# Kernel tuning notes

Hardware: AMD Instinct MI355X
Metric: run time of the kernel (lower is better)

Reference implementation:

```python
import jax, jax.numpy as jnp
from jax import lax
import numpy as np


def setup_inputs() -> dict:
    key = jax.random.key(0)
    k1, k2 = jax.random.split(key)
    sat_features = jax.random.normal(k1, (128, 4, 64, 16), dtype=jnp.float32)  # [B_s, h, w, c]
    grd_features = jax.random.normal(k2, (128, 4, 64, 16), dtype=jnp.float32)  # [B_g, h, gw, c]
    return {"sat_features": sat_features, "grd_features": grd_features}


def reference(sat_features, grd_features):
    B_s, h, w, c = sat_features.shape
    B_g, gh, gw, gc = grd_features.shape
    assert h == gh and c == gc

    # --- corr: circular cross-correlation over width via conv2d ---
    n = gw - 1
    sat_pad = jnp.concatenate([sat_features, sat_features[:, :, :n, :]], axis=2)  # [B_s,h,w+n,c]
    rhs = jnp.transpose(grd_features, (1, 2, 3, 0))  # HWIO: [h,gw,c,B_g]
    out = lax.conv_general_dilated(
        sat_pad, rhs, window_strides=(1, 1), padding='VALID',
        dimension_numbers=('NHWC', 'HWIO', 'NHWC'))  # [B_s,1,w,B_g]
    corr = out[:, 0, :, :]                  # [B_s, w, B_g]
    orien = jnp.argmax(corr, axis=1)        # [B_s, B_g] int

    # --- crop_sat: circular-shift gather along width, crop to grd width ---
    shift = orien % w                                                   # [B_s,B_g]
    idx = (jnp.arange(gw)[None, None, :] + shift[:, :, None]) % w       # [B_s,B_g,gw]
    # gather: sat_crop[i,j,y,k,ch] = sat_features[i, y, idx[i,j,k], ch]
    sat_crop = jnp.take_along_axis(
        sat_features[:, None],              # [B_s,1,h,w,c]
        idx[:, :, None, :, None],           # [B_s,B_g,1,gw,1]
        axis=3)                             # -> [B_s,B_g,h,gw,c]

    # --- L2 normalize per (sat,grd) pair and squared-chord distance ---
    norm = jnp.sqrt(jnp.sum(sat_crop * sat_crop, axis=(2, 3, 4), keepdims=True))
    sat_matrix = sat_crop / jnp.maximum(norm, 1e-12)
    dot = jnp.sum(sat_matrix * grd_features[None], axis=(2, 3, 4))      # [B_s,B_g]
    distance = 2.0 - 2.0 * dot.T                                        # [B_g,B_s]

    return sat_features, grd_features, distance, orien
```

## Files before the change

kernel.cpp:

```cpp
#include <hip/hip_runtime.h>
#include <math.h>

typedef _Float16 f16;
typedef __attribute__((ext_vector_type(8))) _Float16 f16x8;
typedef __attribute__((ext_vector_type(16))) float f32x16;

#define DIST_OFF  1048576
#define ORI_OFF   1064960
#define SATP_STR  72

#define MFMA(a,b,c) __builtin_amdgcn_mfma_f32_32x32x16_f16((a),(b),(c),0,0,0)

__global__ __launch_bounds__(256) void prep_k(const float* __restrict__ grd,
                                              f16* __restrict__ gHi, f16* __restrict__ gLo) {
    const int b = blockIdx.x;
    __shared__ f16 tH[8192], tL[8192];
    const int tid = threadIdx.x;
    const int g0 = (b & 7) * 16;
    const int kq = b >> 3;
    #pragma unroll
    for (int i = 0; i < 32; ++i) {
        int flat = i * 256 + tid;
        int g_l = flat >> 9;
        int r   = flat & 511;
        int h   = r >> 7;
        int j   = r & 127;
        float v = grd[(((g0 + g_l) * 4 + h) * 64 + kq * 8) * 16 + j];
        int k_l = (j >> 4) * 64 + h * 16 + (j & 15);
        f16 hv = (f16)v;
        int a = (k_l >> 3) * 128 + g_l * 8 + (k_l & 7);
        tH[a] = hv;
        tL[a] = (f16)(v - (float)hv);
    }
    __syncthreads();
    #pragma unroll
    for (int i = 0; i < 4; ++i) {
        int f = i * 256 + tid;
        int dst = (kq * 64 + (f >> 4)) * 128 + g0 + (f & 15);
        ((f16x8*)gHi)[dst] = *(const f16x8*)(tH + f * 8);
        ((f16x8*)gLo)[dst] = *(const f16x8*)(tL + f * 8);
    }
}

__global__ __launch_bounds__(512, 4) void corr_k(const float* __restrict__ sat,
                                                 const f16* __restrict__ gHi,
                                                 const f16* __restrict__ gLo,
                                                 float* __restrict__ out,
                                                 const float4* __restrict__ satIn,
                                                 const float4* __restrict__ grdIn,
                                                 float4* __restrict__ out4,
                                                 int doCopy) {
    __shared__ __align__(16) unsigned char smem[65536];
    __shared__ float wred[8];
    __shared__ float rnormS;
    f16* sH = (f16*)smem;
    f16* sL = sH + 127 * SATP_STR;
    float* red = (float*)smem;

    const int tid = threadIdx.x;
    const int s  = blockIdx.x >> 2;
    const int gq = blockIdx.x & 3;
    const int wave = tid >> 6, lane = tid & 63;
    const int m = lane & 31, half = lane >> 5;

    const float* satS = sat + s * 4096;
    float ssq = 0.f;
    #pragma unroll
    for (int r = 0; r < 8; ++r) {
        int idx = r * 512 + tid;
        float v = satS[idx];
        int h = idx >> 10, w = (idx >> 4) & 63, c = idx & 15;
        int col = h * 16 + c;
        f16 hv = (f16)v, lv = (f16)(v - (float)hv);
        sH[w * SATP_STR + col] = hv;
        sL[w * SATP_STR + col] = lv;
        if (w < 63) { sH[(w + 64) * SATP_STR + col] = hv; sL[(w + 64) * SATP_STR + col] = lv; }
        ssq += v * v;
    }
    #pragma unroll
    for (int off = 32; off > 0; off >>= 1) ssq += __shfl_down(ssq, off, 64);
    if (lane == 0) wred[wave] = ssq;
    __syncthreads();
    if (tid == 0) {
        float t = 0.f;
        #pragma unroll
        for (int i = 0; i < 8; ++i) t += wred[i];
        rnormS = 1.f / fmaxf(sqrtf(t), 1e-12f);
    }

    const f16* A0h = sH + m * SATP_STR + half * 8;
    const f16* A0l = sL + m * SATP_STR + half * 8;
    const f16x8* BHp = (const f16x8*)gHi;
    const f16x8* BLp = (const f16x8*)gLo;
    const int bBase = half * 128 + gq * 32 + m;

    f32x16 z;
    #pragma unroll
    for (int r = 0; r < 16; ++r) z[r] = 0.f;
    f32x16 h0 = z, h1 = z, x0 = z, x1 = z;

    f16x8 a0h, a0l, a1h, a1l, bh[2], bl[2];

#define LOADB(p, t) { int bu = (t) * 256 + bBase; bh[p] = BHp[bu]; bl[p] = BLp[bu]; }
#define LOADA(t) { int ao = ((t) >> 2) * SATP_STR + ((t) & 3) * 16; \
    a0h = *(const f16x8*)(A0h + ao); a0l = *(const f16x8*)(A0l + ao); \
    a1h = *(const f16x8*)(A0h + ao + 32 * SATP_STR); \
    a1l = *(const f16x8*)(A0l + ao + 32 * SATP_STR); }

    const int t0 = wave * 32;
    LOADB(0, t0)
    #pragma unroll
    for (int tt = 0; tt < 32; ++tt) {
        if (tt < 31) LOADB((tt + 1) & 1, t0 + tt + 1)
        LOADA(t0 + tt)
        h0 = MFMA(a0h, bh[tt & 1], h0);
        h1 = MFMA(a1h, bh[tt & 1], h1);
        x0 = MFMA(a0h, bl[tt & 1], x0); x0 = MFMA(a0l, bh[tt & 1], x0);
        x1 = MFMA(a1h, bl[tt & 1], x1); x1 = MFMA(a1l, bh[tt & 1], x1);
    }
    f32x16 p0 = h0 + x0, p1 = h1 + x1;

    __syncthreads();
    float* rw = red + wave * 2048;
    #pragma unroll
    for (int r = 0; r < 16; ++r) {
        int j0 = (r & 3) + 8 * (r >> 2) + 4 * half;
        rw[j0 * 32 + m]        = p0[r];
        rw[(j0 + 32) * 32 + m] = p1[r];
    }
    __syncthreads();
    #pragma unroll
    for (int i = 0; i < 4; ++i) {
        int c = i * 512 + tid;
        float v = red[c]          + red[c + 2048]  + red[c + 4096]  + red[c + 6144]
                + red[c + 8192]   + red[c + 10240] + red[c + 12288] + red[c + 14336];
        red[c] = v;
    }
    __syncthreads();

    if (tid < 32) {
        int g = tid;
        float best = red[g];
        int bj = 0;
        for (int j = 1; j < 64; ++j) {
            float v = red[j * 32 + g];
            if (v > best) { best = v; bj = j; }
        }
        float dot = best * rnormS;
        int gg = gq * 32 + g;
        out[DIST_OFF + gg * 128 + s] = 2.f - 2.f * dot;
        out[ORI_OFF + s * 128 + gg]  = (float)bj;
    }

    if (doCopy) {
        int i = blockIdx.x * 512 + tid;
        out4[i] = (i < 131072) ? satIn[i] : grdIn[i - 131072];
    }
}

__global__ void copy_k(const float4* __restrict__ a, const float4* __restrict__ b,
                       float4* __restrict__ out) {
    int i = blockIdx.x * 256 + threadIdx.x;
    out[i] = a[i];
    out[131072 + i] = b[i];
}

extern "C" void kernel_launch(void* const* d_in, const int* in_sizes, int n_in,
                              void* d_out, int out_size, void* d_ws, size_t ws_size,
                              hipStream_t stream) {
    const float* sat = (const float*)d_in[0];
    const float* grd = (const float*)d_in[1];
    float* out = (float*)d_out;

    const bool useWs = (ws_size >= (size_t)2 * 1024 * 1024);
    f16* gHi;
    f16* gLo;
    if (useWs) {
        gHi = (f16*)d_ws;
        gLo = gHi + 524288;
    } else {
        gHi = (f16*)out;
        gLo = (f16*)(out + 262144);
    }

    prep_k<<<64, 256, 0, stream>>>(grd, gHi, gLo);
    corr_k<<<512, 512, 0, stream>>>(sat, gHi, gLo, out,
                                    (const float4*)sat, (const float4*)grd, (float4*)out,
                                    useWs ? 1 : 0);
    if (!useWs)
        copy_k<<<512, 256, 0, stream>>>((const float4*)sat, (const float4*)grd, (float4*)out);
}
```

Before: 86.88 us.

## Use single fp16 MFMA pass with exact fp32 rescoring of near-max candidates

Drops the hi/lo split-fp16 compensation, so the correlation GEMM issues one MFMA per tile instead of three and loads half the A and B data. To keep argmax and distance accurate, each wave now takes a block-wide max per ground column, picks candidate shifts within a fixed margin of it, and recomputes their dot products in fp32 from global memory. It also prefetches A fragments with double buffering. The rescoring loop is data dependent and adds global reads, and a candidate outside the margin could be missed.

Result: slower. 104.3 us (+20.0%).

```diff
diff --git a/kernel.cpp b/kernel.cpp
--- a/kernel.cpp
+++ b/kernel.cpp
@@ -12,9 +12,9 @@
 #define MFMA(a,b,c) __builtin_amdgcn_mfma_f32_32x32x16_f16((a),(b),(c),0,0,0)
 
 __global__ __launch_bounds__(256) void prep_k(const float* __restrict__ grd,
-                                              f16* __restrict__ gHi, f16* __restrict__ gLo) {
+                                              f16* __restrict__ gHi) {
     const int b = blockIdx.x;
-    __shared__ f16 tH[8192], tL[8192];
+    __shared__ f16 tH[8192];
     const int tid = threadIdx.x;
     const int g0 = (b & 7) * 16;
     const int kq = b >> 3;
@@ -27,10 +27,7 @@
         int j   = r & 127;
         float v = grd[(((g0 + g_l) * 4 + h) * 64 + kq * 8) * 16 + j];
         int k_l = (j >> 4) * 64 + h * 16 + (j & 15);
-        f16 hv = (f16)v;
-        int a = (k_l >> 3) * 128 + g_l * 8 + (k_l & 7);
-        tH[a] = hv;
-        tL[a] = (f16)(v - (float)hv);
+        tH[(k_l >> 3) * 128 + g_l * 8 + (k_l & 7)] = (f16)v;
     }
     __syncthreads();
     #pragma unroll
@@ -38,13 +35,12 @@
         int f = i * 256 + tid;
         int dst = (kq * 64 + (f >> 4)) * 128 + g0 + (f & 15);
         ((f16x8*)gHi)[dst] = *(const f16x8*)(tH + f * 8);
-        ((f16x8*)gLo)[dst] = *(const f16x8*)(tL + f * 8);
     }
 }
 
 __global__ __launch_bounds__(512, 4) void corr_k(const float* __restrict__ sat,
+                                                 const float* __restrict__ grd,
                                                  const f16* __restrict__ gHi,
-                                                 const f16* __restrict__ gLo,
                                                  float* __restrict__ out,
                                                  const float4* __restrict__ satIn,
                                                  const float4* __restrict__ grdIn,
@@ -54,7 +50,6 @@
     __shared__ float wred[8];
     __shared__ float rnormS;
     f16* sH = (f16*)smem;
-    f16* sL = sH + 127 * SATP_STR;
     float* red = (float*)smem;
 
     const int tid = threadIdx.x;
@@ -71,10 +66,9 @@
         float v = satS[idx];
         int h = idx >> 10, w = (idx >> 4) & 63, c = idx & 15;
         int col = h * 16 + c;
-        f16 hv = (f16)v, lv = (f16)(v - (float)hv);
+        f16 hv = (f16)v;
         sH[w * SATP_STR + col] = hv;
-        sL[w * SATP_STR + col] = lv;
-        if (w < 63) { sH[(w + 64) * SATP_STR + col] = hv; sL[(w + 64) * SATP_STR + col] = lv; }
+        if (w < 63) sH[(w + 64) * SATP_STR + col] = hv;
         ssq += v * v;
     }
     #pragma unroll
@@ -89,44 +83,37 @@
     }
 
     const f16* A0h = sH + m * SATP_STR + half * 8;
-    const f16* A0l = sL + m * SATP_STR + half * 8;
     const f16x8* BHp = (const f16x8*)gHi;
-    const f16x8* BLp = (const f16x8*)gLo;
     const int bBase = half * 128 + gq * 32 + m;
 
     f32x16 z;
     #pragma unroll
     for (int r = 0; r < 16; ++r) z[r] = 0.f;
-    f32x16 h0 = z, h1 = z, x0 = z, x1 = z;
-
-    f16x8 a0h, a0l, a1h, a1l, bh[2], bl[2];
-
-#define LOADB(p, t) { int bu = (t) * 256 + bBase; bh[p] = BHp[bu]; bl[p] = BLp[bu]; }
-#define LOADA(t) { int ao = ((t) >> 2) * SATP_STR + ((t) & 3) * 16; \
-    a0h = *(const f16x8*)(A0h + ao); a0l = *(const f16x8*)(A0l + ao); \
-    a1h = *(const f16x8*)(A0h + ao + 32 * SATP_STR); \
-    a1l = *(const f16x8*)(A0l + ao + 32 * SATP_STR); }
+    f32x16 h0 = z, h1 = z;
+
+    f16x8 a0[2], a1[2], bh[2];
+
+#define LOADB(p, t) { int bu = (t) * 256 + bBase; bh[p] = BHp[bu]; }
+#define LOADA(p, t) { int ao = ((t) >> 2) * SATP_STR + ((t) & 3) * 16; \
+    a0[p] = *(const f16x8*)(A0h + ao); \
+    a1[p] = *(const f16x8*)(A0h + ao + 32 * SATP_STR); }
 
     const int t0 = wave * 32;
-    LOADB(0, t0)
+    LOADA(0, t0) LOADB(0, t0)
     #pragma unroll
     for (int tt = 0; tt < 32; ++tt) {
-        if (tt < 31) LOADB((tt + 1) & 1, t0 + tt + 1)
-        LOADA(t0 + tt)
-        h0 = MFMA(a0h, bh[tt & 1], h0);
-        h1 = MFMA(a1h, bh[tt & 1], h1);
-        x0 = MFMA(a0h, bl[tt & 1], x0); x0 = MFMA(a0l, bh[tt & 1], x0);
-        x1 = MFMA(a1h, bl[tt & 1], x1); x1 = MFMA(a1l, bh[tt & 1], x1);
-    }
-    f32x16 p0 = h0 + x0, p1 = h1 + x1;
+        if (tt < 31) { LOADA((tt + 1) & 1, t0 + tt + 1) LOADB((tt + 1) & 1, t0 + tt + 1) }
+        h0 = MFMA(a0[tt & 1], bh[tt & 1], h0);
+        h1 = MFMA(a1[tt & 1], bh[tt & 1], h1);
+    }
 
     __syncthreads();
     float* rw = red + wave * 2048;
     #pragma unroll
     for (int r = 0; r < 16; ++r) {
         int j0 = (r & 3) + 8 * (r >> 2) + 4 * half;
-        rw[j0 * 32 + m]        = p0[r];
-        rw[(j0 + 32) * 32 + m] = p1[r];
+        rw[j0 * 32 + m]        = h0[r];
+        rw[(j0 + 32) * 32 + m] = h1[r];
     }
     __syncthreads();
     #pragma unroll
@@ -138,18 +125,42 @@
     }
     __syncthreads();
 
-    if (tid < 32) {
-        int g = tid;
-        float best = red[g];
-        int bj = 0;
-        for (int j = 1; j < 64; ++j) {
-            float v = red[j * 32 + g];
-            if (v > best) { best = v; bj = j; }
+    const float* gBase = grd + (gq * 32) * 4096;
+    #pragma unroll
+    for (int i = 0; i < 4; ++i) {
+        int g = wave * 4 + i;
+        float v = red[lane * 32 + g];
+        float mx = v;
+        #pragma unroll
+        for (int off = 32; off > 0; off >>= 1) mx = fmaxf(mx, __shfl_xor(mx, off, 64));
+        unsigned long long mask = __ballot(v >= mx - 3.0f);
+        float bestDot = -3.4e38f; int bj = 0;
+        while (mask) {
+            int j = __ffsll((long long)mask) - 1;
+            mask &= mask - 1;
+            int wsat = (lane + j) & 63;
+            const float* gp = gBase + g * 4096;
+            float acc = 0.f;
+            #pragma unroll
+            for (int h = 0; h < 4; ++h) {
+                const float4* s4 = (const float4*)(satS + h * 1024 + wsat * 16);
+                const float4* g4 = (const float4*)(gp  + h * 1024 + lane * 16);
+                #pragma unroll
+                for (int q = 0; q < 4; ++q) {
+                    float4 a = s4[q], b = g4[q];
+                    acc += a.x * b.x; acc += a.y * b.y; acc += a.z * b.z; acc += a.w * b.w;
+                }
+            }
+            #pragma unroll
+            for (int off = 32; off > 0; off >>= 1) acc += __shfl_xor(acc, off, 64);
+            if (acc > bestDot) { bestDot = acc; bj = j; }
         }
-        float dot = best * rnormS;
-        int gg = gq * 32 + g;
-        out[DIST_OFF + gg * 128 + s] = 2.f - 2.f * dot;
-        out[ORI_OFF + s * 128 + gg]  = (float)bj;
+        if (lane == 0) {
+            float dot = bestDot * rnormS;
+            int gg = gq * 32 + g;
+            out[DIST_OFF + gg * 128 + s] = 2.f - 2.f * dot;
+            out[ORI_OFF + s * 128 + gg]  = (float)bj;
+        }
     }
 
     if (doCopy) {
@@ -172,19 +183,16 @@
     const float* grd = (const float*)d_in[1];
     float* out = (float*)d_out;
 
-    const bool useWs = (ws_size >= (size_t)2 * 1024 * 1024);
+    const bool useWs = (ws_size >= (size_t)1024 * 1024 * 2);
     f16* gHi;
-    f16* gLo;
     if (useWs) {
         gHi = (f16*)d_ws;
-        gLo = gHi + 524288;
     } else {
         gHi = (f16*)out;
-        gLo = (f16*)(out + 262144);
-    }
-
-    prep_k<<<64, 256, 0, stream>>>(grd, gHi, gLo);
-    corr_k<<<512, 512, 0, stream>>>(sat, gHi, gLo, out,
+    }
+
+    prep_k<<<64, 256, 0, stream>>>(grd, gHi);
+    corr_k<<<512, 512, 0, stream>>>(sat, grd, gHi, out,
                                     (const float4*)sat, (const float4*)grd, (float4*)out,
                                     useWs ? 1 : 0);
     if (!useWs)
```
